# Performance work log

Hardware: AMD Instinct MI355X
Metric: run time of the kernel (lower is better)

Reference implementation:

```python
import jax, jax.numpy as jnp
import numpy as np

B, N, T, D = 256, 12, 20, 512
EPS_A = 1e-6          # adjacency row-sum epsilon (matches torch code)
EPS_BN = 1e-5         # BatchNorm2d default eps
DIST_THRESH = 150.0   # pixel distance threshold for graph edges


def setup_inputs() -> dict:
    key = jax.random.key(0)
    ks = jax.random.split(key, 16)
    person_features = jax.random.normal(ks[0], (B, N, T, D), dtype=jnp.float32)
    # bboxes: (x, y, w, h) in pixel coordinates of a 1280x720 frame
    bboxes = jax.random.uniform(ks[1], (B, N, 4), dtype=jnp.float32) \
             * jnp.array([1280.0, 720.0, 120.0, 200.0], dtype=jnp.float32)
    inp = {"person_features": person_features, "bboxes": bboxes}
    # STGCN layer params: 1x1 conv == per-node linear [D_out, D_in], plus BN affine + running stats
    for li in (1, 2):
        k = jax.random.split(ks[1 + li], 6)
        inp[f"W{li}"] = jax.random.normal(k[0], (D, D), dtype=jnp.float32) * (1.0 / np.sqrt(D))
        inp[f"b{li}"] = jax.random.normal(k[1], (D,), dtype=jnp.float32) * 0.01
        inp[f"g{li}"] = jnp.ones((D,), dtype=jnp.float32) + 0.1 * jax.random.normal(k[2], (D,), dtype=jnp.float32)
        inp[f"beta{li}"] = 0.1 * jax.random.normal(k[3], (D,), dtype=jnp.float32)
        inp[f"m{li}"] = 0.1 * jax.random.normal(k[4], (D,), dtype=jnp.float32)
        inp[f"v{li}"] = 0.5 + jax.random.uniform(k[5], (D,), dtype=jnp.float32)
    return inp


def _stgcn(x, A_norm, W, b, g, beta, m, v):
    # x: [B, N, C]; A_norm: [B, N, N] row-normalized adjacency
    # torch: out[c, j] = sum_n x[n, c] * A_norm[n, j]
    xg = jnp.einsum('bnc,bnj->bjc', x, A_norm)           # graph aggregation
    y = xg @ W.T + b                                      # 1x1 conv over channels
    y = g * (y - m) * jax.lax.rsqrt(v + EPS_BN) + beta    # BatchNorm2d (inference)
    return jax.nn.relu(y)


def reference(person_features, bboxes, W1, b1, g1, beta1, m1, v1,
              W2, b2, g2, beta2, m2, v2):
    # box centers: (x + w/2, y + h/2)  -> [B, N, 2]
    centers = jnp.stack([bboxes[..., 0] + bboxes[..., 2] * 0.5,
                         bboxes[..., 1] + bboxes[..., 3] * 0.5], axis=-1)
    # squared pairwise distance (threshold on d^2 avoids sqrt-at-zero); diag d=0<150 -> 1,
    # identical to off-diag threshold + added identity in the torch code.
    diff = centers[:, :, None, :] - centers[:, None, :, :]   # [B, N, N, 2]
    d2 = jnp.sum(diff * diff, axis=-1)                       # [B, N, N]
    A = (d2 < DIST_THRESH * DIST_THRESH).astype(jnp.float32)
    A_norm = A / (jnp.sum(A, axis=-1, keepdims=True) + EPS_A)

    x = person_features[:, :, -1, :]                         # last timestep [B, N, D]
    x = _stgcn(x, A_norm, W1, b1, g1, beta1, m1, v1)
    x = _stgcn(x, A_norm, W2, b2, g2, beta2, m2, v2)
    # write enhanced features back into the last timestep
    return person_features.at[:, :, -1, :].set(x)
```

## Files before the change

### kernel.cpp

```cpp
#include <hip/hip_runtime.h>

#define BB 256
#define NP 12
#define TT 20
#define DD 512
#define EPS_A 1e-6f
#define EPS_BN 1e-5f
#define THR2 (150.0f * 150.0f)
#define APITCH 520
#define NSLICE 2432u
#define TOTALC 7471104u
#define CSPLIT 2990080u
#define NCOPY1 2016
#define NCOPY2 256

typedef __attribute__((ext_vector_type(8))) short shortx8;
typedef __attribute__((ext_vector_type(4))) float floatx4;

static __device__ __forceinline__ ushort f2bf(float f) {
    unsigned x = __float_as_uint(f);
    return (ushort)((x + 0x7fffu + ((x >> 16) & 1u)) >> 16);
}

static __device__ __forceinline__ void copy_span(uint lo, uint hi, uint tid, uint cb,
                                                 uint ncb, uint tpb,
                                                 const float4* __restrict__ src,
                                                 float4* __restrict__ dst) {
    uint step = ncb * tpb * 8u;
    for (uint i0 = lo + (cb * tpb + tid) * 8u; i0 < hi; i0 += step) {
        uint g = i0 / NSLICE;
        uint idx = i0 + g * 128u;
        float4 v0 = src[idx + 0], v1 = src[idx + 1], v2 = src[idx + 2], v3 = src[idx + 3];
        float4 v4 = src[idx + 4], v5 = src[idx + 5], v6 = src[idx + 6], v7 = src[idx + 7];
        dst[idx + 0] = v0; dst[idx + 1] = v1; dst[idx + 2] = v2; dst[idx + 3] = v3;
        dst[idx + 4] = v4; dst[idx + 5] = v5; dst[idx + 6] = v6; dst[idx + 7] = v7;
    }
}

__global__ __launch_bounds__(256) void k_copyprep(
    const float* __restrict__ W1, const float* __restrict__ W2,
    const float* __restrict__ b1, const float* __restrict__ g1,
    const float* __restrict__ beta1, const float* __restrict__ m1, const float* __restrict__ v1,
    const float* __restrict__ b2, const float* __restrict__ g2,
    const float* __restrict__ beta2, const float* __restrict__ m2, const float* __restrict__ v2,
    float* __restrict__ s1, float* __restrict__ t1, float* __restrict__ s2, float* __restrict__ t2,
    ushort* __restrict__ wb1, ushort* __restrict__ wb2,
    const float4* __restrict__ csrc, float4* __restrict__ cdst) {
    int bid = blockIdx.x, t = threadIdx.x;
    if (bid < 64) {
        int idx = bid * 256 + t;
        #pragma unroll 2
        for (int i = idx; i < 131072; i += 16384) {
            float4 f = (i < 65536) ? ((const float4*)W1)[i] : ((const float4*)W2)[i - 65536];
            ushort4 u;
            u.x = f2bf(f.x); u.y = f2bf(f.y); u.z = f2bf(f.z); u.w = f2bf(f.w);
            if (i < 65536) *(ushort4*)(wb1 + (long)i * 4) = u;
            else           *(ushort4*)(wb2 + (long)(i - 65536) * 4) = u;
        }
    } else if (bid == 64) {
        for (int d = t; d < DD; d += 256) {
            float sa = g1[d] * rsqrtf(v1[d] + EPS_BN);
            s1[d] = sa; t1[d] = (b1[d] - m1[d]) * sa + beta1[d];
            float sb = g2[d] * rsqrtf(v2[d] + EPS_BN);
            s2[d] = sb; t2[d] = (b2[d] - m2[d]) * sb + beta2[d];
        }
    } else {
        copy_span(CSPLIT, TOTALC, t, bid - 65, NCOPY1, 256, csrc, cdst);
    }
}

template <int LAYER>
static __device__ __forceinline__ void gemm8w(
    int wave, int lane, int b,
    const ushort (*__restrict__ xgl)[APITCH], float (*__restrict__ y1l)[DD],
    const ushort* __restrict__ wb, const float* __restrict__ sv, const float* __restrict__ tv,
    float* __restrict__ outp) {
    int mrow = lane & 15, quad = lane >> 4;
    floatx4 acc[4];
    #pragma unroll
    for (int nt = 0; nt < 4; nt++) acc[nt] = (floatx4){0.f, 0.f, 0.f, 0.f};

    const ushort* wbase = wb + ((long)(wave * 64 + mrow)) * DD + quad * 8;
    #pragma unroll 4
    for (int kc = 0; kc < DD; kc += 32) {
        shortx8 af = *(const shortx8*)&xgl[mrow][kc + quad * 8];
        #pragma unroll
        for (int nt = 0; nt < 4; nt++) {
            shortx8 bf = *(const shortx8*)(wbase + nt * 16 * DD + kc);
            acc[nt] = __builtin_amdgcn_mfma_f32_16x16x32_bf16(af, bf, acc[nt], 0, 0, 0);
        }
    }

    #pragma unroll
    for (int nt = 0; nt < 4; nt++) {
        int d = wave * 64 + nt * 16 + mrow;
        float s = sv[d], tt = tv[d];
        #pragma unroll
        for (int v = 0; v < 4; v++) {
            int m = quad * 4 + v;
            float val = fmaxf(acc[nt][v] * s + tt, 0.f);
            if (m < NP) {
                if (LAYER == 1) y1l[m][d] = val;
                else outp[((long)(b * NP + m) * TT + (TT - 1)) * DD + d] = val;
            }
        }
    }
}

__global__ __launch_bounds__(512, 4) void k_compute(
    const float* __restrict__ pf, const float* __restrict__ bboxes,
    const ushort* __restrict__ wb1, const ushort* __restrict__ wb2,
    const float* __restrict__ s1, const float* __restrict__ t1,
    const float* __restrict__ s2, const float* __restrict__ t2,
    float* __restrict__ out,
    const float4* __restrict__ csrc, float4* __restrict__ cdst) {
    __shared__ float cx[NP], cy[NP], Ash[NP][NP], rinv[NP], at[NP][NP];
    __shared__ __align__(16) ushort xgl[16][APITCH];
    __shared__ float y1l[NP][DD];

    int bid = blockIdx.x, t = threadIdx.x;
    if (bid >= BB) {
        copy_span(0u, CSPLIT, t, bid - BB, NCOPY2, 512, csrc, cdst);
        return;
    }

    int b = bid;
    int lane = t & 63, wave = t >> 6;

    if (t < NP) {
        const float* p = bboxes + (b * NP + t) * 4;
        cx[t] = p[0] + 0.5f * p[2];
        cy[t] = p[1] + 0.5f * p[3];
    }
    {
        uint* xz = (uint*)&xgl[NP][0];
        for (int i = t; i < 4 * APITCH / 2; i += 512) xz[i] = 0;
    }
    __syncthreads();
    if (t < NP * NP) {
        int n = t / NP, k = t % NP;
        float dx = cx[n] - cx[k], dy = cy[n] - cy[k];
        Ash[n][k] = (dx * dx + dy * dy < THR2) ? 1.f : 0.f;
    }
    __syncthreads();
    if (t < NP) {
        float s = 0.f;
        #pragma unroll
        for (int k = 0; k < NP; k++) s += Ash[t][k];
        rinv[t] = 1.f / (s + EPS_A);
    }
    __syncthreads();
    if (t < NP * NP) {
        int j = t / NP, n = t % NP;
        at[j][n] = Ash[n][j] * rinv[n];
    }
    __syncthreads();

    for (int c = t; c < DD; c += 512) {
        float xv[NP];
        #pragma unroll
        for (int n = 0; n < NP; n++)
            xv[n] = pf[((long)((b * NP + n) * TT + TT - 1)) * DD + c];
        #pragma unroll
        for (int j = 0; j < NP; j++) {
            float a = 0.f;
            #pragma unroll
            for (int n = 0; n < NP; n++) a += at[j][n] * xv[n];
            xgl[j][c] = f2bf(a);
        }
    }
    __syncthreads();

    gemm8w<1>(wave, lane, b, xgl, y1l, wb1, s1, t1, nullptr);
    __syncthreads();

    for (int c = t; c < DD; c += 512) {
        float xv[NP];
        #pragma unroll
        for (int n = 0; n < NP; n++) xv[n] = y1l[n][c];
        #pragma unroll
        for (int j = 0; j < NP; j++) {
            float a = 0.f;
            #pragma unroll
            for (int n = 0; n < NP; n++) a += at[j][n] * xv[n];
            xgl[j][c] = f2bf(a);
        }
    }
    __syncthreads();

    gemm8w<2>(wave, lane, b, xgl, y1l, wb2, s2, t2, out);
}

extern "C" void kernel_launch(void* const* d_in, const int* in_sizes, int n_in,
                              void* d_out, int out_size, void* d_ws, size_t ws_size,
                              hipStream_t stream) {
    const float* pf = (const float*)d_in[0];
    const float* bboxes = (const float*)d_in[1];
    const float* W1 = (const float*)d_in[2];
    const float* b1 = (const float*)d_in[3];
    const float* g1 = (const float*)d_in[4];
    const float* beta1 = (const float*)d_in[5];
    const float* m1 = (const float*)d_in[6];
    const float* v1 = (const float*)d_in[7];
    const float* W2 = (const float*)d_in[8];
    const float* b2 = (const float*)d_in[9];
    const float* g2 = (const float*)d_in[10];
    const float* beta2 = (const float*)d_in[11];
    const float* m2 = (const float*)d_in[12];
    const float* v2 = (const float*)d_in[13];
    float* out = (float*)d_out;

    float* ws = (float*)d_ws;
    float* s1 = ws;
    float* t1v = ws + 512;
    float* s2 = ws + 1024;
    float* t2v = ws + 1536;
    ushort* wb1 = (ushort*)(ws + 2048);
    ushort* wb2 = wb1 + 262144;

    const float4* csrc = (const float4*)pf;
    float4* cdst = (float4*)out;

    k_copyprep<<<65 + NCOPY1, 256, 0, stream>>>(W1, W2, b1, g1, beta1, m1, v1,
                                                b2, g2, beta2, m2, v2,
                                                s1, t1v, s2, t2v, wb1, wb2, csrc, cdst);
    k_compute<<<BB + NCOPY2, 512, 0, stream>>>(pf, bboxes, wb1, wb2,
                                               s1, t1v, s2, t2v, out, csrc, cdst);
}
```

Measured before the change: 293.1 us.

## Rework passthrough copy into per-float4 strided loop and rebalance copy split

Replaces the 8-float4-per-thread copy over compacted indices with a simple grid-stride loop over every float4 of the output, skipping rows that are the last timestep. The split moves most of the copy (three quarters) into the first kernel and raises block counts for both the copy and the weight-to-bf16 conversion. The aim is simpler addressing and better load balance between the two launches. The cost is one float4 per iteration, less memory-level parallelism per thread, and a branch that idles lanes on every 20th row.

```diff
diff --git a/kernel.cpp b/kernel.cpp
--- a/kernel.cpp
+++ b/kernel.cpp
@@ -8,11 +8,10 @@
 #define EPS_BN 1e-5f
 #define THR2 (150.0f * 150.0f)
 #define APITCH 520
-#define NSLICE 2432u
-#define TOTALC 7471104u
-#define CSPLIT 2990080u
-#define NCOPY1 2016
-#define NCOPY2 256
+#define CTOTAL 7864320L
+#define K2LO   5898240L
+#define NCPY1 2048
+#define NCPY2 1024
 
 typedef __attribute__((ext_vector_type(8))) short shortx8;
 typedef __attribute__((ext_vector_type(4))) float floatx4;
@@ -22,18 +21,14 @@
     return (ushort)((x + 0x7fffu + ((x >> 16) & 1u)) >> 16);
 }
 
-static __device__ __forceinline__ void copy_span(uint lo, uint hi, uint tid, uint cb,
-                                                 uint ncb, uint tpb,
+static __device__ __forceinline__ void copy_body(int cb, int ncb, int tpb, long lo, long hi,
                                                  const float4* __restrict__ src,
                                                  float4* __restrict__ dst) {
-    uint step = ncb * tpb * 8u;
-    for (uint i0 = lo + (cb * tpb + tid) * 8u; i0 < hi; i0 += step) {
-        uint g = i0 / NSLICE;
-        uint idx = i0 + g * 128u;
-        float4 v0 = src[idx + 0], v1 = src[idx + 1], v2 = src[idx + 2], v3 = src[idx + 3];
-        float4 v4 = src[idx + 4], v5 = src[idx + 5], v6 = src[idx + 6], v7 = src[idx + 7];
-        dst[idx + 0] = v0; dst[idx + 1] = v1; dst[idx + 2] = v2; dst[idx + 3] = v3;
-        dst[idx + 4] = v4; dst[idx + 5] = v5; dst[idx + 6] = v6; dst[idx + 7] = v7;
+    long stride = (long)ncb * tpb;
+    for (long g = lo + (long)cb * tpb + threadIdx.x; g < hi; g += stride) {
+        int row = (int)(g >> 7);
+        if (row % TT == TT - 1) continue;
+        dst[g] = src[g];
     }
 }
 
@@ -47,17 +42,18 @@
     ushort* __restrict__ wb1, ushort* __restrict__ wb2,
     const float4* __restrict__ csrc, float4* __restrict__ cdst) {
     int bid = blockIdx.x, t = threadIdx.x;
-    if (bid < 64) {
+    if (bid < 128) {
         int idx = bid * 256 + t;
-        #pragma unroll 2
-        for (int i = idx; i < 131072; i += 16384) {
+        #pragma unroll
+        for (int k = 0; k < 4; k++) {
+            int i = idx + k * 32768;
             float4 f = (i < 65536) ? ((const float4*)W1)[i] : ((const float4*)W2)[i - 65536];
             ushort4 u;
             u.x = f2bf(f.x); u.y = f2bf(f.y); u.z = f2bf(f.z); u.w = f2bf(f.w);
             if (i < 65536) *(ushort4*)(wb1 + (long)i * 4) = u;
             else           *(ushort4*)(wb2 + (long)(i - 65536) * 4) = u;
         }
-    } else if (bid == 64) {
+    } else if (bid == 128) {
         for (int d = t; d < DD; d += 256) {
             float sa = g1[d] * rsqrtf(v1[d] + EPS_BN);
             s1[d] = sa; t1[d] = (b1[d] - m1[d]) * sa + beta1[d];
@@ -65,7 +61,7 @@
             s2[d] = sb; t2[d] = (b2[d] - m2[d]) * sb + beta2[d];
         }
     } else {
-        copy_span(CSPLIT, TOTALC, t, bid - 65, NCOPY1, 256, csrc, cdst);
+        copy_body(bid - 129, NCPY1, 256, 0L, K2LO, csrc, cdst);
     }
 }
 
@@ -120,7 +116,7 @@
 
     int bid = blockIdx.x, t = threadIdx.x;
     if (bid >= BB) {
-        copy_span(0u, CSPLIT, t, bid - BB, NCOPY2, 512, csrc, cdst);
+        copy_body(bid - BB, NCPY2, 512, K2LO, CTOTAL, csrc, cdst);
         return;
     }
 
@@ -221,9 +217,9 @@
     const float4* csrc = (const float4*)pf;
     float4* cdst = (float4*)out;
 
-    k_copyprep<<<65 + NCOPY1, 256, 0, stream>>>(W1, W2, b1, g1, beta1, m1, v1,
+    k_copyprep<<<129 + NCPY1, 256, 0, stream>>>(W1, W2, b1, g1, beta1, m1, v1,
                                                 b2, g2, beta2, m2, v2,
                                                 s1, t1v, s2, t2v, wb1, wb2, csrc, cdst);
-    k_compute<<<BB + NCOPY2, 512, 0, stream>>>(pf, bboxes, wb1, wb2,
-                                               s1, t1v, s2, t2v, out, csrc, cdst);
-}
+    k_compute<<<BB + NCPY2, 512, 0, stream>>>(pf, bboxes, wb1, wb2,
+                                              s1, t1v, s2, t2v, out, csrc, cdst);
+}
```

Measured after the change: 274.1 us. 1.07x faster.
